# Kernel tuning notes

Hardware: AMD Instinct MI355X
Metric: run time of the kernel (lower is better)

The kernel has to match this reference:

```python
import jax, jax.numpy as jnp
import numpy as np

T, N, E, F_IN, C = 8, 50000, 800000, 64, 64


def setup_inputs() -> dict:
    key = jax.random.key(0)
    ks = jax.random.split(key, 32)
    inp = {
        "x": jax.random.normal(ks[0], (T, N, F_IN), dtype=jnp.float32),
        "edge_index": jax.random.randint(ks[1], (2, E), 0, N, dtype=jnp.int32),
        "edge_weight": jax.random.uniform(ks[2], (E,), dtype=jnp.float32),
    }
    s = 0.05
    names = ["xz", "hz", "xr", "hr", "xh", "hh"]
    for i, nm in enumerate(names):
        cin = F_IN if nm[0] == "x" else C
        inp[f"W{nm}0"] = jax.random.normal(ks[3 + 3 * i], (cin, C), dtype=jnp.float32) * s
        inp[f"W{nm}1"] = jax.random.normal(ks[4 + 3 * i], (cin, C), dtype=jnp.float32) * s
        inp[f"b{nm}"] = jax.random.normal(ks[5 + 3 * i], (C,), dtype=jnp.float32) * s
    inp["W_lin"] = jax.random.normal(ks[30], (C, 1), dtype=jnp.float32) * s
    inp["b_lin"] = jax.random.normal(ks[31], (1,), dtype=jnp.float32) * s
    return inp


def reference(x, edge_index, edge_weight,
              Wxz0, Wxz1, bxz, Whz0, Whz1, bhz,
              Wxr0, Wxr1, bxr, Whr0, Whr1, bhr,
              Wxh0, Wxh1, bxh, Whh0, Whh1, bhh,
              W_lin, b_lin):
    src, dst = edge_index[0], edge_index[1]
    n = x.shape[1]
    # sym-normalized L_hat = -D^{-1/2} A D^{-1/2} (ChebConv, lambda_max=2)
    deg = jnp.zeros((n,), x.dtype).at[src].add(edge_weight)
    dinv = jnp.where(deg > 0, jax.lax.rsqrt(jnp.maximum(deg, 1e-12)), 0.0)
    nw = -edge_weight * dinv[src] * dinv[dst]  # (E,)

    def cheb(v, W0, W1, b):
        # K=2 Chebyshev: v @ W0 + (L_hat v) @ W1 + b ; v: (T, N, Cin)
        msgs = nw[None, :, None] * v[:, src, :]          # (T, E, Cin)
        tx1 = jnp.zeros_like(v).at[:, dst, :].add(msgs)  # scatter-add over nodes
        return v @ W0 + tx1 @ W1 + b

    H = jnp.zeros(x.shape[:2] + (Whz0.shape[0],), x.dtype)  # H=None -> zeros
    Z = jax.nn.sigmoid(cheb(x, Wxz0, Wxz1, bxz) + cheb(H, Whz0, Whz1, bhz))
    R = jax.nn.sigmoid(cheb(x, Wxr0, Wxr1, bxr) + cheb(H, Whr0, Whr1, bhr))
    Ht = jnp.tanh(cheb(x, Wxh0, Wxh1, bxh) + cheb(R * H, Whh0, Whh1, bhh))
    H = Z * H + (1.0 - Z) * Ht
    h = jax.nn.relu(H)
    return h @ W_lin + b_lin
```

## Files before the change

kernel.cpp:

```cpp
#include <hip/hip_runtime.h>

#define T_ 8
#define N_ 50000
#define E_ 800000
#define C_ 64
#define OVF_CAP 131072
#define NB 196
#define NBLK 256
#define EPB 3125
#define SCN (2 * NB * NBLK)
#define SCAN_TILES 49

typedef __attribute__((ext_vector_type(8))) short bf16x8;
typedef __attribute__((ext_vector_type(4))) float f32x4;

__device__ inline short f2bf(float f) {
    union { float f; unsigned int u; } v; v.f = f;
    unsigned int u = v.u + 0x7FFFu + ((v.u >> 16) & 1u);
    return (short)(u >> 16);
}
__device__ inline float bf2f_lo(unsigned int u) {
    union { unsigned int u; float f; } v; v.u = u << 16;
    return v.f;
}
__device__ inline float bf2f_hi(unsigned int u) {
    union { unsigned int u; float f; } v; v.u = u & 0xffff0000u;
    return v.f;
}

__device__ inline void xcvt_step(int id, const float* __restrict__ x,
                                 unsigned short* __restrict__ xb) {
    int c8 = id & 7;
    int t = (id >> 3) & 7;
    int n = id >> 6;
    const float* xr = x + ((long long)t * N_ + n) * C_ + c8 * 8;
    float4 a = *(const float4*)(xr);
    float4 b = *(const float4*)(xr + 4);
    bf16x8 o;
    o[0] = f2bf(a.x); o[1] = f2bf(a.y); o[2] = f2bf(a.z); o[3] = f2bf(a.w);
    o[4] = f2bf(b.x); o[5] = f2bf(b.y); o[6] = f2bf(b.z); o[7] = f2bf(b.w);
    *(bf16x8*)(xb + (long long)id * 8) = o;
}

__global__ __launch_bounds__(256) void prep_kernel(
        const int* __restrict__ src, const int* __restrict__ dst,
        int* __restrict__ counts,
        const float* __restrict__ x, unsigned short* __restrict__ xb,
        const float* __restrict__ Wz0, const float* __restrict__ Wz1,
        const float* __restrict__ Wh0, const float* __restrict__ Wh1,
        short* __restrict__ swz) {
    if (blockIdx.x < NBLK) {
        __shared__ int h[2 * NB];
        int t = threadIdx.x;
        for (int i = t; i < 2 * NB; i += 256) h[i] = 0;
        __syncthreads();
        int e0 = blockIdx.x * EPB;
        for (int j = t; j < EPB; j += 256) {
            int e = e0 + j;
            atomicAdd(&h[src[e] >> 8], 1);
            atomicAdd(&h[NB + (dst[e] >> 8)], 1);
        }
        __syncthreads();
        for (int i = t; i < 2 * NB; i += 256)
            counts[i * NBLK + blockIdx.x] = h[i];
    } else if (blockIdx.x < NBLK + 12500) {
        int id = (blockIdx.x - NBLK) * 256 + threadIdx.x;
        xcvt_step(id, x, xb);
    } else {
        int idx = (blockIdx.x - NBLK - 12500) * 256 + threadIdx.x;
        int j = idx & 7;
        int lane = (idx >> 3) & 63;
        int kb = (idx >> 9) & 1;
        int c = (idx >> 10) & 3;
        int mat = idx >> 12;
        const float* W = (mat == 0) ? Wz0 : (mat == 1) ? Wz1 : (mat == 2) ? Wh0 : Wh1;
        int k = kb * 32 + (lane >> 4) * 8 + j;
        int n = c * 16 + (lane & 15);
        swz[idx] = f2bf(W[k * 64 + n]);
    }
}

__global__ __launch_bounds__(1024) void scan_a_kernel(int* __restrict__ cnts,
                                                      int* __restrict__ tsum) {
    __shared__ int wsum[16];
    int tid = threadIdx.x, lane = tid & 63, wid = tid >> 6;
    int i0 = blockIdx.x * 2048 + tid * 2;
    int v0 = cnts[i0], v1 = cnts[i0 + 1];
    int orig = v0 + v1;
    int v = orig;
#pragma unroll
    for (int off = 1; off < 64; off <<= 1) {
        int u = __shfl_up(v, off);
        if (lane >= off) v += u;
    }
    if (lane == 63) wsum[wid] = v;
    __syncthreads();
    if (wid == 0) {
        int s = (lane < 16) ? wsum[lane] : 0;
#pragma unroll
        for (int off = 1; off < 16; off <<= 1) {
            int u = __shfl_up(s, off);
            if (lane >= off) s += u;
        }
        if (lane < 16) wsum[lane] = s;
    }
    __syncthreads();
    int wpre = wid ? wsum[wid - 1] : 0;
    int ex = wpre + v - orig;
    cnts[i0] = ex;
    cnts[i0 + 1] = ex + v0;
    if (tid == 0) tsum[blockIdx.x] = wsum[15];
}

__global__ __launch_bounds__(1024) void scan_b_kernel(const int* __restrict__ tsum,
                                                      int* __restrict__ cnts) {
    __shared__ int soff[SCAN_TILES];
    int tid = threadIdx.x, lane = tid & 63, wid = tid >> 6;
    if (wid == 0) {
        int own = (lane < SCAN_TILES) ? tsum[lane] : 0;
        int s = own;
#pragma unroll
        for (int off = 1; off < 64; off <<= 1) {
            int u = __shfl_up(s, off);
            if (lane >= off) s += u;
        }
        if (lane < SCAN_TILES) soff[lane] = s - own;
    }
    __syncthreads();
    int off = soff[blockIdx.x];
    int i0 = blockIdx.x * 2048 + tid;
    cnts[i0] += off;
    cnts[i0 + 1024] += off;
}

__global__ __launch_bounds__(256) void scatter_kernel(
        const int* __restrict__ src, const int* __restrict__ dst,
        const float* __restrict__ w, const int* __restrict__ scn,
        int2* __restrict__ rec) {
    __shared__ int offs[2 * NB];
    int t = threadIdx.x;
    for (int i = t; i < 2 * NB; i += 256)
        offs[i] = scn[i * NBLK + blockIdx.x];
    __syncthreads();
    int e0 = blockIdx.x * EPB;
    for (int j = t; j < EPB; j += 256) {
        int e = e0 + j;
        int s = src[e], d = dst[e];
        float wv = w[e];
        int r0 = atomicAdd(&offs[s >> 8], 1);
        rec[r0] = make_int2(s, __float_as_int(wv));
        int r1 = atomicAdd(&offs[NB + (d >> 8)], 1);
        rec[r1] = make_int2(s | ((d & 255) << 16), __float_as_int(wv));
    }
}

__global__ __launch_bounds__(256) void degw_kernel(
        const int2* __restrict__ rec, const int* __restrict__ scn,
        float* __restrict__ degw) {
    __shared__ float acc[256];
    int t = threadIdx.x, b = blockIdx.x;
    acc[t] = 0.f;
    __syncthreads();
    int s0 = scn[b * NBLK];
    int s1 = (b == NB - 1) ? E_ : scn[(b + 1) * NBLK];
    for (int j = s0 + t; j < s1; j += 256) {
        int2 r = rec[j];
        atomicAdd(&acc[r.x & 255], __int_as_float(r.y));
    }
    __syncthreads();
    int node = b * 256 + t;
    if (node < N_) degw[node] = acc[t];
}

__global__ __launch_bounds__(256) void esbuild_kernel(
        const int2* __restrict__ rec, const int* __restrict__ scn,
        const float* __restrict__ degw, int* __restrict__ cnt,
        int2* __restrict__ es, int cap,
        int* __restrict__ ovfcnt, int4* __restrict__ ovf) {
    __shared__ int cl[256];
    __shared__ float di[256];
    int t = threadIdx.x, b = blockIdx.x;
    cl[t] = 0;
    int node = b * 256 + t;
    float dd = (node < N_) ? degw[node] : 0.f;
    di[t] = dd > 0.f ? rsqrtf(fmaxf(dd, 1e-12f)) : 0.f;
    __syncthreads();
    int s0 = scn[(NB + b) * NBLK];
    int s1 = (b == NB - 1) ? 2 * E_ : scn[(NB + b + 1) * NBLK];
    for (int j = s0 + t; j < s1; j += 256) {
        int2 r = rec[j];
        int s = r.x & 0xffff;
        int dl = (r.x >> 16) & 255;
        float ds = degw[s];
        float is = ds > 0.f ? rsqrtf(fmaxf(ds, 1e-12f)) : 0.f;
        float nwv = -__int_as_float(r.y) * is * di[dl];
        int rank = atomicAdd(&cl[dl], 1);
        int d = b * 256 + dl;
        if (rank < cap) {
            es[d * cap + rank] = make_int2(s, __float_as_int(nwv));
        } else {
            int op = atomicAdd(ovfcnt, 1);
            if (op < OVF_CAP) ovf[op] = make_int4(d, s, __float_as_int(nwv), 0);
        }
    }
    __syncthreads();
    if (node < N_) cnt[node] = cl[t];
}

#define ACC8(W, V)                                                       \
    acc[0] += (W) * bf2f_lo((V).x); acc[1] += (W) * bf2f_hi((V).x);      \
    acc[2] += (W) * bf2f_lo((V).y); acc[3] += (W) * bf2f_hi((V).y);      \
    acc[4] += (W) * bf2f_lo((V).z); acc[5] += (W) * bf2f_hi((V).z);      \
    acc[6] += (W) * bf2f_lo((V).w); acc[7] += (W) * bf2f_hi((V).w);

__global__ __launch_bounds__(256) void gather_node_kernel(
        const int* __restrict__ cnt, const int2* __restrict__ es, int cap,
        const int* __restrict__ ovfcnt, const int4* __restrict__ ovf,
        const unsigned short* __restrict__ xb, const short* __restrict__ swz,
        const float* __restrict__ bxz, const float* __restrict__ bhz,
        const float* __restrict__ bxh, const float* __restrict__ bhh,
        const float* __restrict__ Wlin, const float* __restrict__ blin,
        float* __restrict__ out) {
    __shared__ unsigned short ltx[32 * 72];
    __shared__ float laz[2][16][65];

    int lane = threadIdx.x & 63;
    int wid = threadIdx.x >> 6;
    int base = blockIdx.x * 4;

    {
        int d = base + wid;
        int t = lane >> 3;
        int oct = lane & 7;
        int2 pk = (lane < cap) ? es[d * cap + lane] : make_int2(0, 0);
        int m = cnt[d];
        int mb = m < cap ? m : cap;

        float acc[8] = {0.f, 0.f, 0.f, 0.f, 0.f, 0.f, 0.f, 0.f};
        const unsigned short* xbase = xb + lane * 8;
        int k = 0;
        for (; k + 3 < mb; k += 4) {
            int s0 = __shfl(pk.x, k);
            int s1 = __shfl(pk.x, k + 1);
            int s2 = __shfl(pk.x, k + 2);
            int s3 = __shfl(pk.x, k + 3);
            uint4 v0 = *(const uint4*)(xbase + (long long)s0 * 512);
            uint4 v1 = *(const uint4*)(xbase + (long long)s1 * 512);
            uint4 v2 = *(const uint4*)(xbase + (long long)s2 * 512);
            uint4 v3 = *(const uint4*)(xbase + (long long)s3 * 512);
            float w0 = __int_as_float(__shfl(pk.y, k));
            float w1 = __int_as_float(__shfl(pk.y, k + 1));
            float w2 = __int_as_float(__shfl(pk.y, k + 2));
            float w3 = __int_as_float(__shfl(pk.y, k + 3));
            ACC8(w0, v0);
            ACC8(w1, v1);
            ACC8(w2, v2);
            ACC8(w3, v3);
        }
        for (; k < mb; ++k) {
            int s0 = __shfl(pk.x, k);
            float w0 = __int_as_float(__shfl(pk.y, k));
            uint4 v0 = *(const uint4*)(xbase + (long long)s0 * 512);
            ACC8(w0, v0);
        }
        if (m > cap) {
            int oc = *ovfcnt;
            if (oc > OVF_CAP) oc = OVF_CAP;
            for (int i = 0; i < oc; ++i) {
                int4 o = ovf[i];
                if (o.x == d) {
                    float w0 = __int_as_float(o.z);
                    uint4 v0 = *(const uint4*)(xbase + (long long)o.y * 512);
                    ACC8(w0, v0);
                }
            }
        }
        uint4 ob;
        ob.x = (unsigned int)(unsigned short)f2bf(acc[0]) |
               ((unsigned int)(unsigned short)f2bf(acc[1]) << 16);
        ob.y = (unsigned int)(unsigned short)f2bf(acc[2]) |
               ((unsigned int)(unsigned short)f2bf(acc[3]) << 16);
        ob.z = (unsigned int)(unsigned short)f2bf(acc[4]) |
               ((unsigned int)(unsigned short)f2bf(acc[5]) << 16);
        ob.w = (unsigned int)(unsigned short)f2bf(acc[6]) |
               ((unsigned int)(unsigned short)f2bf(acc[7]) << 16);
        int r = wid * 8 + t;
        *(uint4*)(ltx + r * 72 + oct * 8) = ob;
    }
    __syncthreads();

    int mt = wid >> 1;
    int g = wid & 1;
    int c16 = lane & 15;
    int kq = lane >> 4;
    int r_blk = mt * 16 + c16;
    const unsigned short* xr = xb + (long long)(base * 8 + r_blk) * C_ + kq * 8;
    bf16x8 ax0 = *(const bf16x8*)(xr);
    bf16x8 ax1 = *(const bf16x8*)(xr + 32);
    bf16x8 at0 = *(const bf16x8*)(ltx + r_blk * 72 + kq * 8);
    bf16x8 at1 = *(const bf16x8*)(ltx + r_blk * 72 + 32 + kq * 8);

    const float* bA = g ? bxh : bxz;
    const float* bB = g ? bhh : bhz;
    const short* wA = swz + (2 * g) * 4096 + lane * 8;
    const short* wB = swz + (2 * g + 1) * 4096 + lane * 8;

    f32x4 a4[4];
#pragma unroll
    for (int c = 0; c < 4; ++c) {
        int col = c * 16 + c16;
        float bv = bA[col] + bB[col];
        a4[c] = (f32x4){bv, bv, bv, bv};
    }
#pragma unroll
    for (int c = 0; c < 4; ++c) {
        bf16x8 bA0 = *(const bf16x8*)(wA + (c * 2 + 0) * 512);
        bf16x8 bA1 = *(const bf16x8*)(wA + (c * 2 + 1) * 512);
        bf16x8 bB0 = *(const bf16x8*)(wB + (c * 2 + 0) * 512);
        bf16x8 bB1 = *(const bf16x8*)(wB + (c * 2 + 1) * 512);
        a4[c] = __builtin_amdgcn_mfma_f32_16x16x32_bf16(ax0, bA0, a4[c], 0, 0, 0);
        a4[c] = __builtin_amdgcn_mfma_f32_16x16x32_bf16(ax1, bA1, a4[c], 0, 0, 0);
        a4[c] = __builtin_amdgcn_mfma_f32_16x16x32_bf16(at0, bB0, a4[c], 0, 0, 0);
        a4[c] = __builtin_amdgcn_mfma_f32_16x16x32_bf16(at1, bB1, a4[c], 0, 0, 0);
    }

    if (g == 0) {
#pragma unroll
        for (int c = 0; c < 4; ++c)
#pragma unroll
            for (int r = 0; r < 4; ++r)
                laz[mt][kq * 4 + r][c * 16 + c16] = a4[c][r];
    }
    __syncthreads();
    if (g == 1) {
        float part[4] = {0.f, 0.f, 0.f, 0.f};
#pragma unroll
        for (int c = 0; c < 4; ++c) {
            int col = c * 16 + c16;
            float wl = Wlin[col];
#pragma unroll
            for (int r = 0; r < 4; ++r) {
                float a = laz[mt][kq * 4 + r][col];
                float b = a4[c][r];
                float z = 1.f / (1.f + __expf(-a));
                float aa = fabsf(b);
                float e = __expf(-2.f * aa);
                float ht = copysignf((1.f - e) / (1.f + e), b);
                float h = fmaxf((1.f - z) * ht, 0.f);
                part[r] += h * wl;
            }
        }
#pragma unroll
        for (int m = 1; m <= 8; m <<= 1) {
#pragma unroll
            for (int r = 0; r < 4; ++r) part[r] += __shfl_xor(part[r], m);
        }
        if (c16 == 0) {
            float bl = blin[0];
#pragma unroll
            for (int r = 0; r < 4; ++r) {
                int rb = mt * 16 + kq * 4 + r;
                out[(long long)(rb & 7) * N_ + base + (rb >> 3)] = part[r] + bl;
            }
        }
    }
}

extern "C" void kernel_launch(void* const* d_in, const int* in_sizes, int n_in,
                              void* d_out, int out_size, void* d_ws, size_t ws_size,
                              hipStream_t stream) {
    const float* x    = (const float*)d_in[0];
    const int*   ei   = (const int*)d_in[1];
    const float* w    = (const float*)d_in[2];
    const float* Wxz0 = (const float*)d_in[3];
    const float* Wxz1 = (const float*)d_in[4];
    const float* bxz  = (const float*)d_in[5];
    const float* bhz  = (const float*)d_in[8];
    const float* Wxh0 = (const float*)d_in[15];
    const float* Wxh1 = (const float*)d_in[16];
    const float* bxh  = (const float*)d_in[17];
    const float* bhh  = (const float*)d_in[20];
    const float* Wlin = (const float*)d_in[21];
    const float* blin = (const float*)d_in[22];
    float* out = (float*)d_out;

    const int* src = ei;
    const int* dst = ei + E_;

    char* ws = (char*)d_ws;
    size_t off = 0;
    auto alloc = [&](size_t bytes) {
        char* p = ws + off;
        off = (off + bytes + 511) & ~(size_t)511;
        return p;
    };
    short* swz         = (short*)alloc(4 * 4096 * sizeof(short));
    float* degw        = (float*)alloc((size_t)N_ * 4);
    int*   cnt         = (int*)alloc((size_t)N_ * 4);
    int*   ovfcnt      = (int*)alloc(512);
    int4*  ovf         = (int4*)alloc((size_t)OVF_CAP * 16);
    int*   counts      = (int*)alloc((size_t)SCN * 4);
    int*   tsum        = (int*)alloc((size_t)SCAN_TILES * 4);
    int2*  rec         = (int2*)alloc((size_t)2 * E_ * 8);
    unsigned short* xb = (unsigned short*)alloc((size_t)T_ * N_ * C_ * 2);
    size_t fixed = off;

    int cap = 16;
    for (int c : {64, 48, 32, 24}) {
        if (fixed + (size_t)N_ * c * 8 + 512 <= ws_size) { cap = c; break; }
    }
    int2* es = (int2*)alloc((size_t)N_ * cap * 8);

    hipMemsetAsync(ovfcnt, 0, 4, stream);

    prep_kernel<<<NBLK + 12500 + 64, 256, 0, stream>>>(
        src, dst, counts, x, xb, Wxz0, Wxz1, Wxh0, Wxh1, swz);

    scan_a_kernel<<<SCAN_TILES, 1024, 0, stream>>>(counts, tsum);
    scan_b_kernel<<<SCAN_TILES, 1024, 0, stream>>>(tsum, counts);

    scatter_kernel<<<NBLK, 256, 0, stream>>>(src, dst, w, counts, rec);

    degw_kernel<<<NB, 256, 0, stream>>>(rec, counts, degw);

    esbuild_kernel<<<NB, 256, 0, stream>>>(rec, counts, degw, cnt,
                                           es, cap, ovfcnt, ovf);

    gather_node_kernel<<<N_ / 4, 256, 0, stream>>>(
        cnt, es, cap, ovfcnt, ovf, xb, swz,
        bxz, bhz, bxh, bhh, Wlin, blin, out);
}
```

Measured before the change: 368.1 us.

## Spread x bf16 conversion across graph-build kernels and deepen gather unroll

After: 373.3 us. No clear change (+1.4%).

```diff
diff --git a/kernel.cpp b/kernel.cpp
--- a/kernel.cpp
+++ b/kernel.cpp
@@ -10,6 +10,10 @@
 #define EPB 3125
 #define SCN (2 * NB * NBLK)
 #define SCAN_TILES 49
+#define XC1 4500
+#define XC4 4000
+#define XC5 2000
+#define XC6 2000
 
 typedef __attribute__((ext_vector_type(8))) short bf16x8;
 typedef __attribute__((ext_vector_type(4))) float f32x4;
@@ -63,11 +67,11 @@
         __syncthreads();
         for (int i = t; i < 2 * NB; i += 256)
             counts[i * NBLK + blockIdx.x] = h[i];
-    } else if (blockIdx.x < NBLK + 12500) {
+    } else if (blockIdx.x < NBLK + XC1) {
         int id = (blockIdx.x - NBLK) * 256 + threadIdx.x;
         xcvt_step(id, x, xb);
     } else {
-        int idx = (blockIdx.x - NBLK - 12500) * 256 + threadIdx.x;
+        int idx = (blockIdx.x - NBLK - XC1) * 256 + threadIdx.x;
         int j = idx & 7;
         int lane = (idx >> 3) & 63;
         int kb = (idx >> 9) & 1;
@@ -113,9 +117,11 @@
 }
 
 __global__ __launch_bounds__(1024) void scan_b_kernel(const int* __restrict__ tsum,
-                                                      int* __restrict__ cnts) {
+                                                      int* __restrict__ cnts,
+                                                      int* __restrict__ ovfcnt) {
     __shared__ int soff[SCAN_TILES];
     int tid = threadIdx.x, lane = tid & 63, wid = tid >> 6;
+    if (blockIdx.x == 0 && tid == 0) *ovfcnt = 0;
     if (wid == 0) {
         int own = (lane < SCAN_TILES) ? tsum[lane] : 0;
         int s = own;
@@ -136,75 +142,93 @@
 __global__ __launch_bounds__(256) void scatter_kernel(
         const int* __restrict__ src, const int* __restrict__ dst,
         const float* __restrict__ w, const int* __restrict__ scn,
-        int2* __restrict__ rec) {
-    __shared__ int offs[2 * NB];
-    int t = threadIdx.x;
-    for (int i = t; i < 2 * NB; i += 256)
-        offs[i] = scn[i * NBLK + blockIdx.x];
-    __syncthreads();
-    int e0 = blockIdx.x * EPB;
-    for (int j = t; j < EPB; j += 256) {
-        int e = e0 + j;
-        int s = src[e], d = dst[e];
-        float wv = w[e];
-        int r0 = atomicAdd(&offs[s >> 8], 1);
-        rec[r0] = make_int2(s, __float_as_int(wv));
-        int r1 = atomicAdd(&offs[NB + (d >> 8)], 1);
-        rec[r1] = make_int2(s | ((d & 255) << 16), __float_as_int(wv));
+        int2* __restrict__ rec,
+        const float* __restrict__ x, unsigned short* __restrict__ xb) {
+    if (blockIdx.x < NBLK) {
+        __shared__ int offs[2 * NB];
+        int t = threadIdx.x;
+        for (int i = t; i < 2 * NB; i += 256)
+            offs[i] = scn[i * NBLK + blockIdx.x];
+        __syncthreads();
+        int e0 = blockIdx.x * EPB;
+        for (int j = t; j < EPB; j += 256) {
+            int e = e0 + j;
+            int s = src[e], d = dst[e];
+            float wv = w[e];
+            int r0 = atomicAdd(&offs[s >> 8], 1);
+            rec[r0] = make_int2(s, __float_as_int(wv));
+            int r1 = atomicAdd(&offs[NB + (d >> 8)], 1);
+            rec[r1] = make_int2(s | ((d & 255) << 16), __float_as_int(wv));
+        }
+    } else {
+        int id = (XC1 + blockIdx.x - NBLK) * 256 + threadIdx.x;
+        xcvt_step(id, x, xb);
     }
 }
 
 __global__ __launch_bounds__(256) void degw_kernel(
         const int2* __restrict__ rec, const int* __restrict__ scn,
-        float* __restrict__ degw) {
-    __shared__ float acc[256];
-    int t = threadIdx.x, b = blockIdx.x;
-    acc[t] = 0.f;
-    __syncthreads();
-    int s0 = scn[b * NBLK];
-    int s1 = (b == NB - 1) ? E_ : scn[(b + 1) * NBLK];
-    for (int j = s0 + t; j < s1; j += 256) {
-        int2 r = rec[j];
-        atomicAdd(&acc[r.x & 255], __int_as_float(r.y));
-    }
-    __syncthreads();
-    int node = b * 256 + t;
-    if (node < N_) degw[node] = acc[t];
+        float* __restrict__ degw,
+        const float* __restrict__ x, unsigned short* __restrict__ xb) {
+    if (blockIdx.x < NB) {
+        __shared__ float acc[256];
+        int t = threadIdx.x, b = blockIdx.x;
+        acc[t] = 0.f;
+        __syncthreads();
+        int s0 = scn[b * NBLK];
+        int s1 = (b == NB - 1) ? E_ : scn[(b + 1) * NBLK];
+        for (int j = s0 + t; j < s1; j += 256) {
+            int2 r = rec[j];
+            atomicAdd(&acc[r.x & 255], __int_as_float(r.y));
+        }
+        __syncthreads();
+        int node = b * 256 + t;
+        if (node < N_) degw[node] = acc[t];
+    } else {
+        int id = (XC1 + XC4 + blockIdx.x - NB) * 256 + threadIdx.x;
+        xcvt_step(id, x, xb);
+    }
 }
 
 __global__ __launch_bounds__(256) void esbuild_kernel(
         const int2* __restrict__ rec, const int* __restrict__ scn,
         const float* __restrict__ degw, int* __restrict__ cnt,
         int2* __restrict__ es, int cap,
-        int* __restrict__ ovfcnt, int4* __restrict__ ovf) {
-    __shared__ int cl[256];
-    __shared__ float di[256];
-    int t = threadIdx.x, b = blockIdx.x;
-    cl[t] = 0;
-    int node = b * 256 + t;
-    float dd = (node < N_) ? degw[node] : 0.f;
-    di[t] = dd > 0.f ? rsqrtf(fmaxf(dd, 1e-12f)) : 0.f;
-    __syncthreads();
-    int s0 = scn[(NB + b) * NBLK];
-    int s1 = (b == NB - 1) ? 2 * E_ : scn[(NB + b + 1) * NBLK];
-    for (int j = s0 + t; j < s1; j += 256) {
-        int2 r = rec[j];
-        int s = r.x & 0xffff;
-        int dl = (r.x >> 16) & 255;
-        float ds = degw[s];
-        float is = ds > 0.f ? rsqrtf(fmaxf(ds, 1e-12f)) : 0.f;
-        float nwv = -__int_as_float(r.y) * is * di[dl];
-        int rank = atomicAdd(&cl[dl], 1);
-        int d = b * 256 + dl;
-        if (rank < cap) {
-            es[d * cap + rank] = make_int2(s, __float_as_int(nwv));
-        } else {
-            int op = atomicAdd(ovfcnt, 1);
-            if (op < OVF_CAP) ovf[op] = make_int4(d, s, __float_as_int(nwv), 0);
-        }
-    }
-    __syncthreads();
-    if (node < N_) cnt[node] = cl[t];
+        int* __restrict__ ovfcnt, int4* __restrict__ ovf,
+        const float* __restrict__ x, unsigned short* __restrict__ xb) {
+    if (blockIdx.x < NB) {
+        __shared__ int cl[256];
+        __shared__ float di[256];
+        int t = threadIdx.x, b = blockIdx.x;
+        cl[t] = 0;
+        int node = b * 256 + t;
+        float dd = (node < N_) ? degw[node] : 0.f;
+        di[t] = dd > 0.f ? rsqrtf(fmaxf(dd, 1e-12f)) : 0.f;
+        __syncthreads();
+        int s0 = scn[(NB + b) * NBLK];
+        int s1 = (b == NB - 1) ? 2 * E_ : scn[(NB + b + 1) * NBLK];
+        for (int j = s0 + t; j < s1; j += 256) {
+            int2 r = rec[j];
+            int s = r.x & 0xffff;
+            int dl = (r.x >> 16) & 255;
+            float ds = degw[s];
+            float is = ds > 0.f ? rsqrtf(fmaxf(ds, 1e-12f)) : 0.f;
+            float nwv = -__int_as_float(r.y) * is * di[dl];
+            int rank = atomicAdd(&cl[dl], 1);
+            int d = b * 256 + dl;
+            if (rank < cap) {
+                es[d * cap + rank] = make_int2(s, __float_as_int(nwv));
+            } else {
+                int op = atomicAdd(ovfcnt, 1);
+                if (op < OVF_CAP) ovf[op] = make_int4(d, s, __float_as_int(nwv), 0);
+            }
+        }
+        __syncthreads();
+        if (node < N_) cnt[node] = cl[t];
+    } else {
+        int id = (XC1 + XC4 + XC5 + blockIdx.x - NB) * 256 + threadIdx.x;
+        xcvt_step(id, x, xb);
+    }
 }
 
 #define ACC8(W, V)                                                       \
@@ -239,6 +263,21 @@
         float acc[8] = {0.f, 0.f, 0.f, 0.f, 0.f, 0.f, 0.f, 0.f};
         const unsigned short* xbase = xb + lane * 8;
         int k = 0;
+        for (; k + 7 < mb; k += 8) {
+            int ss[8];
+#pragma unroll
+            for (int j = 0; j < 8; ++j) ss[j] = __shfl(pk.x, k + j);
+            uint4 vv[8];
+#pragma unroll
+            for (int j = 0; j < 8; ++j)
+                vv[j] = *(const uint4*)(xbase + (long long)ss[j] * 512);
+            float ww[8];
+#pragma unroll
+            for (int j = 0; j < 8; ++j)
+                ww[j] = __int_as_float(__shfl(pk.y, k + j));
+#pragma unroll
+            for (int j = 0; j < 8; ++j) { ACC8(ww[j], vv[j]); }
+        }
         for (; k + 3 < mb; k += 4) {
             int s0 = __shfl(pk.x, k);
             int s1 = __shfl(pk.x, k + 1);
@@ -411,20 +450,18 @@
     }
     int2* es = (int2*)alloc((size_t)N_ * cap * 8);
 
-    hipMemsetAsync(ovfcnt, 0, 4, stream);
-
-    prep_kernel<<<NBLK + 12500 + 64, 256, 0, stream>>>(
+    prep_kernel<<<NBLK + XC1 + 64, 256, 0, stream>>>(
         src, dst, counts, x, xb, Wxz0, Wxz1, Wxh0, Wxh1, swz);
 
     scan_a_kernel<<<SCAN_TILES, 1024, 0, stream>>>(counts, tsum);
-    scan_b_kernel<<<SCAN_TILES, 1024, 0, stream>>>(tsum, counts);
-
-    scatter_kernel<<<NBLK, 256, 0, stream>>>(src, dst, w, counts, rec);
-
-    degw_kernel<<<NB, 256, 0, stream>>>(rec, counts, degw);
-
-    esbuild_kernel<<<NB, 256, 0, stream>>>(rec, counts, degw, cnt,
-                                           es, cap, ovfcnt, ovf);
+    scan_b_kernel<<<SCAN_TILES, 1024, 0, stream>>>(tsum, counts, ovfcnt);
+
+    scatter_kernel<<<NBLK + XC4, 256, 0, stream>>>(src, dst, w, counts, rec, x, xb);
+
+    degw_kernel<<<NB + XC5, 256, 0, stream>>>(rec, counts, degw, x, xb);
+
+    esbuild_kernel<<<NB + XC6, 256, 0, stream>>>(rec, counts, degw, cnt,
+                                                 es, cap, ovfcnt, ovf, x, xb);
 
     gather_node_kernel<<<N_ / 4, 256, 0, stream>>>(
         cnt, es, cap, ovfcnt, ovf, xb, swz,
```
